# Kernel tuning notes

Measured on AMD Instinct MI355X. Metric: run time of the kernel, lower is better.

## Reference

```python
import jax, jax.numpy as jnp
import numpy as np

N = 1_000_000
IN_DIM = 256
HIDDEN = 32
NUM_SEG = 100_000


def setup_inputs() -> dict:
    key = jax.random.key(0)
    ks = jax.random.split(key, 6)
    review_x = jax.random.normal(ks[0], (N, IN_DIM), dtype=jnp.float32)
    Wq = jax.random.normal(ks[1], (IN_DIM, HIDDEN), dtype=jnp.float32) * (1.0 / np.sqrt(IN_DIM))
    bq = jax.random.normal(ks[2], (HIDDEN,), dtype=jnp.float32) * 0.01
    Wk = jax.random.normal(ks[3], (IN_DIM, HIDDEN), dtype=jnp.float32) * (1.0 / np.sqrt(IN_DIM))
    bk = jax.random.normal(ks[4], (HIDDEN,), dtype=jnp.float32) * 0.01
    review_to_rest_idx = jax.random.randint(ks[5], (N,), 0, NUM_SEG, dtype=jnp.int64 if jax.config.jax_enable_x64 else jnp.int32)
    return {
        "review_x": review_x,
        "Wq": Wq,
        "bq": bq,
        "Wk": Wk,
        "bk": bk,
        "review_to_rest_idx": review_to_rest_idx,
        "num_segments": NUM_SEG,
    }


def reference(review_x, Wq, bq, Wk, bk, review_to_rest_idx, num_segments):
    # q/k projections: [N, hidden]
    qv = review_x @ Wq + bq
    kv = review_x @ Wk + bk
    # attention logits per review: [N]
    att = jnp.sum(qv * kv, axis=-1)
    idx = review_to_rest_idx
    # segment softmax (numerically stable): max, exp, sum per restaurant group
    seg_max = jax.ops.segment_max(att, idx, num_segments=num_segments)
    # empty segments yield -inf max; never gathered, but keep finite for safety
    seg_max = jnp.where(jnp.isfinite(seg_max), seg_max, 0.0)
    e = jnp.exp(att - seg_max[idx])
    seg_sum = jax.ops.segment_sum(e, idx, num_segments=num_segments)
    weights = e / seg_sum[idx]
    return weights
```

## Files before the change

kernel.cpp:

```cpp
#include <hip/hip_runtime.h>
#include <hip/hip_fp16.h>
#include <math.h>

#define IN_DIM 256
#define HID 32
#define NSEG 100000
#define TROWS 64
#define ROWB 1024

typedef _Float16 half8 __attribute__((ext_vector_type(8)));
typedef __fp16  fp16x2 __attribute__((ext_vector_type(2)));
typedef float floatx4 __attribute__((ext_vector_type(4)));

__device__ __forceinline__ void gload_lds16(const float* g, char* l) {
    __builtin_amdgcn_global_load_lds(
        (const __attribute__((address_space(1))) void*)g,
        (__attribute__((address_space(3))) void*)l,
        16, 0, 0);
}

__global__ __launch_bounds__(256, 2) void att_kernel(
    const float* __restrict__ x,
    const float* __restrict__ Wq, const float* __restrict__ bq,
    const float* __restrict__ Wk, const float* __restrict__ bk,
    const int* __restrict__ idx,
    float* __restrict__ e_out, float* __restrict__ segsum,
    int n, int nt)
{
    extern __shared__ char smem[];

    const int tid = threadIdx.x;
    const int w  = tid >> 6, l = tid & 63;
    const int lr = l & 15,  lg = l >> 4;

    const int nb = gridDim.x, bx = blockIdx.x;
    const int qt = nt / nb, rt = nt % nb;
    const int t0  = bx * qt + (bx < rt ? bx : rt);
    const int ntb = qt + (bx < rt ? 1 : 0);
    if (ntb <= 0) return;

    {
        _Float16* BF = (_Float16*)smem;
        const int ks = tid >> 5, lg2 = (tid >> 3) & 3, j = tid & 7;
        const float4* wqr = (const float4*)(Wq + (size_t)tid * HID);
        const float4* wkr = (const float4*)(Wk + (size_t)tid * HID);
#pragma unroll
        for (int i = 0; i < 8; ++i) {
            float4 vq = wqr[i];
            float4 vk = wkr[i];
            float fq[4] = { vq.x, vq.y, vq.z, vq.w };
            float fk[4] = { vk.x, vk.y, vk.z, vk.w };
#pragma unroll
            for (int u2 = 0; u2 < 4; ++u2) {
                int c = i * 4 + u2, cg = c >> 4, cr = c & 15;
                BF[(((cg    ) * 8 + ks) * 64 + lg2 * 16 + cr) * 8 + j] = (_Float16)fq[u2];
                BF[(((cg + 2) * 8 + ks) * 64 + lg2 * 16 + cr) * 8 + j] = (_Float16)fk[u2];
            }
        }
    }
    __syncthreads();
    half8 b[4][8];
    {
        const _Float16* bfl = (const _Float16*)smem + (size_t)l * 8;
#pragma unroll
        for (int cg = 0; cg < 4; ++cg)
#pragma unroll
            for (int ks = 0; ks < 8; ++ks)
                b[cg][ks] = *(const half8*)(bfl + (cg * 8 + ks) * 512);
    }
    __syncthreads();

    const float bq0 = bq[lr], bq1 = bq[lr + 16];
    const float bk0 = bk[lr], bk1 = bk[lr + 16];

    for (int i = 0; i < ntb; ++i) {
        const int ti = t0 + i;

#pragma unroll
        for (int j = 0; j < 16; ++j) {
            const int row = j * 4 + w;
            int grow = ti * TROWS + row;
            if (grow >= n) grow = n - 1;
            const float* src = x + (size_t)grow * IN_DIM + ((l ^ (row & 7)) << 2);
            gload_lds16(src, smem + row * ROWB);
        }
        __syncthreads();

        floatx4 acc0 = {0.f,0.f,0.f,0.f}, acc1 = {0.f,0.f,0.f,0.f};
        floatx4 acc2 = {0.f,0.f,0.f,0.f}, acc3 = {0.f,0.f,0.f,0.f};
        const char* Xr = smem + (w * 16 + lr) * ROWB;
        const int sw = lr & 7;
#pragma unroll
        for (int ks = 0; ks < 8; ++ks) {
            float4 v0 = *(const float4*)(Xr + ks * 128 + (((lg * 2 + 0) ^ sw) << 4));
            float4 v1 = *(const float4*)(Xr + ks * 128 + (((lg * 2 + 1) ^ sw) << 4));
            union { half8 h8; fp16x2 h2[4]; } u;
            u.h2[0] = __builtin_amdgcn_cvt_pkrtz(v0.x, v0.y);
            u.h2[1] = __builtin_amdgcn_cvt_pkrtz(v0.z, v0.w);
            u.h2[2] = __builtin_amdgcn_cvt_pkrtz(v1.x, v1.y);
            u.h2[3] = __builtin_amdgcn_cvt_pkrtz(v1.z, v1.w);
            acc0 = __builtin_amdgcn_mfma_f32_16x16x32_f16(u.h8, b[0][ks], acc0, 0, 0, 0);
            acc1 = __builtin_amdgcn_mfma_f32_16x16x32_f16(u.h8, b[1][ks], acc1, 0, 0, 0);
            acc2 = __builtin_amdgcn_mfma_f32_16x16x32_f16(u.h8, b[2][ks], acc2, 0, 0, 0);
            acc3 = __builtin_amdgcn_mfma_f32_16x16x32_f16(u.h8, b[3][ks], acc3, 0, 0, 0);
        }

        float p[4];
#pragma unroll
        for (int i2 = 0; i2 < 4; ++i2) {
            p[i2] = (acc0[i2] + bq0) * (acc2[i2] + bk0)
                  + (acc1[i2] + bq1) * (acc3[i2] + bk1);
            p[i2] += __shfl_xor(p[i2], 1);
            p[i2] += __shfl_xor(p[i2], 2);
            p[i2] += __shfl_xor(p[i2], 4);
            p[i2] += __shfl_xor(p[i2], 8);
        }
        if (lr < 4) {
            float pv = (lr & 1) ? ((lr & 2) ? p[3] : p[1])
                                : ((lr & 2) ? p[2] : p[0]);
            int r = ti * TROWS + w * 16 + lg * 4 + lr;
            if (r < n) {
                float e = __expf(pv);
                e_out[r] = e;
                atomicAdd(&segsum[idx[r]], e);
            }
        }
        __syncthreads();
    }
}

__global__ __launch_bounds__(256) void norm_kernel(
    const int* __restrict__ idx, const float* __restrict__ segsum,
    float* __restrict__ out, int n)
{
    int i = blockIdx.x * blockDim.x + threadIdx.x;
    int stride = gridDim.x * blockDim.x;
    int n4 = n >> 2;
    for (; i < n4; i += stride) {
        float4 e = ((const float4*)out)[i];
        int4  s4 = ((const int4*)idx)[i];
        float4 r;
        r.x = e.x / segsum[s4.x];
        r.y = e.y / segsum[s4.y];
        r.z = e.z / segsum[s4.z];
        r.w = e.w / segsum[s4.w];
        ((float4*)out)[i] = r;
    }
    if (blockIdx.x == 0 && threadIdx.x < (n & 3)) {
        int j = (n & ~3) + threadIdx.x;
        out[j] = out[j] / segsum[idx[j]];
    }
}

extern "C" void kernel_launch(void* const* d_in, const int* in_sizes, int n_in,
                              void* d_out, int out_size, void* d_ws, size_t ws_size,
                              hipStream_t stream)
{
    const float* x   = (const float*)d_in[0];
    const float* Wq  = (const float*)d_in[1];
    const float* bq  = (const float*)d_in[2];
    const float* Wk  = (const float*)d_in[3];
    const float* bk  = (const float*)d_in[4];
    const int*   idx = (const int*)d_in[5];
    const int n = in_sizes[5];

    float* segsum = (float*)d_ws;

    (void)hipMemsetAsync(segsum, 0, (size_t)NSEG * 4, stream);

    const int nt = (n + TROWS - 1) / TROWS;
    int grid1 = 512;
    if (grid1 > nt) grid1 = nt;
    att_kernel<<<grid1, 256, 65536, stream>>>(x, Wq, bq, Wk, bk, idx,
                                              (float*)d_out, segsum, n, nt);

    int n4 = n >> 2;
    int grid2 = (n4 + 255) / 256;
    if (grid2 > 1024) grid2 = 1024;
    if (grid2 < 1) grid2 = 1;
    norm_kernel<<<grid2, 256, 0, stream>>>(idx, segsum, (float*)d_out, n);
}
```

Baseline: 224.5 us.

## Give each wavefront its own 16-row tile and prefetch the next tile

```diff
diff --git a/kernel.cpp b/kernel.cpp
--- a/kernel.cpp
+++ b/kernel.cpp
@@ -5,8 +5,8 @@
 #define IN_DIM 256
 #define HID 32
 #define NSEG 100000
-#define TROWS 64
 #define ROWB 1024
+#define WBUF 16384
 
 typedef _Float16 half8 __attribute__((ext_vector_type(8)));
 typedef __fp16  fp16x2 __attribute__((ext_vector_type(2)));
@@ -25,19 +25,13 @@
     const float* __restrict__ Wk, const float* __restrict__ bk,
     const int* __restrict__ idx,
     float* __restrict__ e_out, float* __restrict__ segsum,
-    int n, int nt)
+    int n, int nsub)
 {
     extern __shared__ char smem[];
 
     const int tid = threadIdx.x;
     const int w  = tid >> 6, l = tid & 63;
     const int lr = l & 15,  lg = l >> 4;
-
-    const int nb = gridDim.x, bx = blockIdx.x;
-    const int qt = nt / nb, rt = nt % nb;
-    const int t0  = bx * qt + (bx < rt ? bx : rt);
-    const int ntb = qt + (bx < rt ? 1 : 0);
-    if (ntb <= 0) return;
 
     {
         _Float16* BF = (_Float16*)smem;
@@ -73,23 +67,34 @@
     const float bq0 = bq[lr], bq1 = bq[lr + 16];
     const float bk0 = bk[lr], bk1 = bk[lr + 16];
 
-    for (int i = 0; i < ntb; ++i) {
-        const int ti = t0 + i;
+    char* const Xw = smem + w * WBUF;
+    const char* const Xr = Xw + lr * ROWB;
+    const int sw = lr & 7;
 
+    auto stage = [&](int s) {
 #pragma unroll
-        for (int j = 0; j < 16; ++j) {
-            const int row = j * 4 + w;
-            int grow = ti * TROWS + row;
+        for (int r = 0; r < 16; ++r) {
+            int grow = s * 16 + r;
             if (grow >= n) grow = n - 1;
-            const float* src = x + (size_t)grow * IN_DIM + ((l ^ (row & 7)) << 2);
-            gload_lds16(src, smem + row * ROWB);
+            const float* src = x + (size_t)grow * IN_DIM + ((l ^ (r & 7)) << 2);
+            gload_lds16(src, Xw + r * ROWB);
         }
-        __syncthreads();
+    };
+
+    const int gw      = blockIdx.x * 4 + w;
+    const int gstride = gridDim.x * 4;
+
+    int s = gw;
+    if (s >= nsub) return;
+
+    stage(s);
+
+    while (true) {
+        asm volatile("s_waitcnt vmcnt(0)" ::: "memory");
+        __builtin_amdgcn_sched_barrier(0);
 
         floatx4 acc0 = {0.f,0.f,0.f,0.f}, acc1 = {0.f,0.f,0.f,0.f};
         floatx4 acc2 = {0.f,0.f,0.f,0.f}, acc3 = {0.f,0.f,0.f,0.f};
-        const char* Xr = smem + (w * 16 + lr) * ROWB;
-        const int sw = lr & 7;
 #pragma unroll
         for (int ks = 0; ks < 8; ++ks) {
             float4 v0 = *(const float4*)(Xr + ks * 128 + (((lg * 2 + 0) ^ sw) << 4));
@@ -115,17 +120,27 @@
             p[i2] += __shfl_xor(p[i2], 4);
             p[i2] += __shfl_xor(p[i2], 8);
         }
+
+        const int snext = s + gstride;
+
+        asm volatile("s_waitcnt lgkmcnt(0)" ::: "memory");
+        __builtin_amdgcn_sched_barrier(0);
+
+        if (snext < nsub) stage(snext);
+
         if (lr < 4) {
             float pv = (lr & 1) ? ((lr & 2) ? p[3] : p[1])
                                 : ((lr & 2) ? p[2] : p[0]);
-            int r = ti * TROWS + w * 16 + lg * 4 + lr;
+            int r = s * 16 + lg * 4 + lr;
             if (r < n) {
                 float e = __expf(pv);
                 e_out[r] = e;
                 atomicAdd(&segsum[idx[r]], e);
             }
         }
-        __syncthreads();
+
+        if (snext >= nsub) break;
+        s = snext;
     }
 }
 
@@ -168,11 +183,11 @@
 
     (void)hipMemsetAsync(segsum, 0, (size_t)NSEG * 4, stream);
 
-    const int nt = (n + TROWS - 1) / TROWS;
+    const int nsub = (n + 15) >> 4;
     int grid1 = 512;
-    if (grid1 > nt) grid1 = nt;
+    if (grid1 * 4 > nsub) grid1 = (nsub + 3) / 4;
     att_kernel<<<grid1, 256, 65536, stream>>>(x, Wq, bq, Wk, bk, idx,
-                                              (float*)d_out, segsum, n, nt);
+                                              (float*)d_out, segsum, n, nsub);
 
     int n4 = n >> 2;
     int grid2 = (n4 + 255) / 256;
```

Result: no change. 222.6 us (-0.8%).
